# Optimization experiments

Hardware: AMD Instinct MI355X
Metric: run time of the kernel (lower is better)

Reference implementation:

```python
import jax, jax.numpy as jnp
import numpy as np

V, T, E, H, B, S = 50000, 45, 256, 512, 32, 256


def setup_inputs() -> dict:
    key = jax.random.key(0)
    ks = jax.random.split(key, 14)
    s = 0.05
    return dict(
        x=jax.random.randint(ks[0], (B, S), 0, V),
        tags=jax.random.randint(ks[1], (B, S), 0, T),
        mask=jnp.ones((B, S), dtype=bool),
        emb=jax.random.normal(ks[2], (V, E), jnp.float32),
        Wih_f=jax.random.normal(ks[3], (4 * H, E), jnp.float32) * s,
        Whh_f=jax.random.normal(ks[4], (4 * H, H), jnp.float32) * s,
        bih_f=jnp.zeros((4 * H,), jnp.float32),
        bhh_f=jnp.zeros((4 * H,), jnp.float32),
        Wih_b=jax.random.normal(ks[5], (4 * H, E), jnp.float32) * s,
        Whh_b=jax.random.normal(ks[6], (4 * H, H), jnp.float32) * s,
        bih_b=jnp.zeros((4 * H,), jnp.float32),
        bhh_b=jnp.zeros((4 * H,), jnp.float32),
        Wout=jax.random.normal(ks[7], (T, 2 * H), jnp.float32) * s,
        bout=jnp.zeros((T,), jnp.float32),
        start=jax.random.normal(ks[8], (T,), jnp.float32) * 0.1,
        end=jax.random.normal(ks[9], (T,), jnp.float32) * 0.1,
        trans=jax.random.normal(ks[10], (T, T), jnp.float32) * 0.1,
    )


def _lstm_dir(xp, Whh, reverse):
    # xp: [S, B, 4H] precomputed input projection + biases; gate order i,f,g,o (torch)
    Bn = xp.shape[1]
    Hn = Whh.shape[1]
    def step(carry, g_in):
        h, c = carry
        g = g_in + h @ Whh.T
        i, f, gg, o = jnp.split(g, 4, axis=-1)
        c = jax.nn.sigmoid(f) * c + jax.nn.sigmoid(i) * jnp.tanh(gg)
        h = jax.nn.sigmoid(o) * jnp.tanh(c)
        return (h, c), h
    init = (jnp.zeros((Bn, Hn), xp.dtype), jnp.zeros((Bn, Hn), xp.dtype))
    _, hs = jax.lax.scan(step, init, xp, reverse=reverse)
    return hs  # [S, B, H]


def _crf_nll(emissions, tags, mask, start, end, trans):
    # emissions: [B, S, T]; neg mean log-likelihood (torchcrf, reduction='mean')
    mf = mask.astype(emissions.dtype)
    em_tag = jnp.take_along_axis(emissions, tags[:, :, None], axis=2)[:, :, 0]  # [B,S]
    num = start[tags[:, 0]] + em_tag[:, 0]
    num = num + ((trans[tags[:, :-1], tags[:, 1:]] + em_tag[:, 1:]) * mf[:, 1:]).sum(1)
    seq_ends = mf.sum(1).astype(tags.dtype) - 1
    last_tags = jnp.take_along_axis(tags, seq_ends[:, None], axis=1)[:, 0]
    num = num + end[last_tags]
    def denom_step(alpha, inp):
        em_t, m_t = inp  # [B,T], [B]
        nxt = jax.nn.logsumexp(alpha[:, :, None] + trans[None, :, :] + em_t[:, None, :], axis=1)
        return jnp.where(m_t[:, None] > 0, nxt, alpha), None
    alpha0 = start[None, :] + emissions[:, 0]
    em_rest = emissions.transpose(1, 0, 2)[1:]  # [S-1, B, T]
    alpha, _ = jax.lax.scan(denom_step, alpha0, (em_rest, mf.T[1:]))
    logZ = jax.nn.logsumexp(alpha + end[None, :], axis=1)
    return -(num - logZ).mean()


def reference(x, tags, mask, emb, Wih_f, Whh_f, bih_f, bhh_f,
              Wih_b, Whh_b, bih_b, bhh_b, Wout, bout, start, end, trans):
    embeds = emb[x]                      # [B, S, E]
    xs = embeds.transpose(1, 0, 2)       # [S, B, E]
    xp_f = jnp.einsum('sbe,ge->sbg', xs, Wih_f) + bih_f + bhh_f
    hs_f = _lstm_dir(xp_f, Whh_f, False)
    xp_b = jnp.einsum('sbe,ge->sbg', xs, Wih_b) + bih_b + bhh_b
    hs_b = _lstm_dir(xp_b, Whh_b, True)
    hcat = jnp.concatenate([hs_f, hs_b], axis=-1)          # [S, B, 2H]
    emissions = jnp.einsum('sbh,th->sbt', hcat, Wout) + bout
    emissions = emissions.transpose(1, 0, 2)                # [B, S, T]
    return _crf_nll(emissions, tags, mask, start, end, trans)
```

## Files before the change

### kernel.cpp

```cpp
#include <hip/hip_runtime.h>
#include <stdint.h>

#define S_LEN 256
#define B_N 32
#define H_N 512
#define E_N 256
#define T_N 45
#define G4H 2048

typedef unsigned short u16;
typedef unsigned int u32;
typedef u16 u16x8 __attribute__((ext_vector_type(8)));
typedef u16 u16x4 __attribute__((ext_vector_type(4)));
typedef u32 u32x4 __attribute__((ext_vector_type(4)));
typedef __bf16 bf16x8 __attribute__((ext_vector_type(8)));
typedef float f32x4 __attribute__((ext_vector_type(4)));
typedef unsigned long long u64;

#define OFF_ATOK  256ull
#define OFF_WIHF  (OFF_ATOK + 4194304ull)
#define OFF_WIHB  (OFF_WIHF + 1048576ull)
#define OFF_WHHF  (OFF_WIHB + 1048576ull)
#define OFF_WHHB  (OFF_WHHF + 2097152ull)
#define OFF_WOUT  (OFF_WHHB + 2097152ull)
#define OFF_BSF   (OFF_WOUT + 98304ull)
#define OFF_BSB   (OFF_BSF + 8192ull)
#define OFF_XPF   (OFF_BSB + 8192ull)
#define OFF_XPB   (OFF_XPF + 33554432ull)
#define OFF_HSF   (OFF_XPB + 33554432ull)
#define OFF_HSB   (OFF_HSF + 8421376ull)
#define OFF_EM    (OFF_HSB + 8421376ull)
#define OFF_VAL   (OFF_EM + 1572864ull)

__device__ __forceinline__ u16 f2bf(float f) {
  union { float f; unsigned u; } v; v.f = f;
  unsigned r = v.u + 0x7FFFu + ((v.u >> 16) & 1u);
  return (u16)(r >> 16);
}
__device__ __forceinline__ float bf2f(u16 b) {
  union { unsigned u; float f; } v; v.u = ((unsigned)b) << 16;
  return v.f;
}
__device__ __forceinline__ bf16x8 ld8(const u16* p) {
  u16x8 v = *reinterpret_cast<const u16x8*>(p);
  return __builtin_bit_cast(bf16x8, v);
}
__device__ __forceinline__ void st_h8cc(u16* p, u16x4 v) {
  __hip_atomic_store(reinterpret_cast<u64*>(p), __builtin_bit_cast(u64, v),
                     __ATOMIC_RELAXED, __HIP_MEMORY_SCOPE_AGENT);
}
__device__ __forceinline__ u32x4 ld16cc(const u16* p) {
  u32x4 r;
  asm volatile("global_load_dwordx4 %0, %1, off sc0 sc1"
               : "=v"(r) : "v"(p) : "memory");
  return r;
}
__device__ __forceinline__ f32x4 mfma16(bf16x8 a, bf16x8 b, f32x4 c) {
  return __builtin_amdgcn_mfma_f32_16x16x32_bf16(a, b, c, 0, 0, 0);
}
__device__ __forceinline__ float sigm(float x) { return 1.f / (1.f + __expf(-x)); }
__device__ __forceinline__ float tanhf_(float x) {
  float ax = fabsf(x);
  float e = __expf(-2.f * ax);
  float t = 1.f - 2.f * e / (1.f + e);
  return (x < 0.f) ? -t : t;
}
__device__ __forceinline__ float wredmax(float v) {
  #pragma unroll
  for (int m = 1; m < 64; m <<= 1) v = fmaxf(v, __shfl_xor(v, m));
  return v;
}
__device__ __forceinline__ float wredsum(float v) {
  #pragma unroll
  for (int m = 1; m < 64; m <<= 1) v += __shfl_xor(v, m);
  return v;
}

__global__ void k_castA(const int* __restrict__ x, const float* __restrict__ emb,
                        u16* __restrict__ atok) {
  int idx = blockIdx.x * 256 + threadIdx.x;
  int t = idx >> 5;
  int e0 = (idx & 31) << 3;
  int s = t >> 5, b = t & 31;
  int xid = x[b * S_LEN + s];
  const float4* p = reinterpret_cast<const float4*>(emb + (size_t)xid * E_N + e0);
  float4 lo = p[0], hi = p[1];
  u16x8 o;
  o[0] = f2bf(lo.x); o[1] = f2bf(lo.y); o[2] = f2bf(lo.z); o[3] = f2bf(lo.w);
  o[4] = f2bf(hi.x); o[5] = f2bf(hi.y); o[6] = f2bf(hi.z); o[7] = f2bf(hi.w);
  *reinterpret_cast<u16x8*>(atok + (size_t)t * E_N + e0) = o;
}

__global__ void k_castW(const float* __restrict__ WihF, const float* __restrict__ WihB,
                        const float* __restrict__ WhhF, const float* __restrict__ WhhB,
                        const float* __restrict__ Wout,
                        const float* __restrict__ bihF, const float* __restrict__ bhhF,
                        const float* __restrict__ bihB, const float* __restrict__ bhhB,
                        u16* wihf, u16* wihb, u16* whhf, u16* whhb, u16* woutp,
                        float* bsf, float* bsb, u16* hsf, u16* hsb) {
  int i = blockIdx.x * 256 + threadIdx.x;
  if (i < 524288) { wihf[i] = f2bf(WihF[i]); return; }
  i -= 524288;
  if (i < 524288) { wihb[i] = f2bf(WihB[i]); return; }
  i -= 524288;
  if (i < 1048576) { whhf[i] = f2bf(WhhF[i]); return; }
  i -= 1048576;
  if (i < 1048576) { whhb[i] = f2bf(WhhB[i]); return; }
  i -= 1048576;
  if (i < 49152) {
    int n = i >> 10, k = i & 1023;
    woutp[i] = (n < T_N) ? f2bf(Wout[n * 1024 + k]) : (u16)0;
    return;
  }
  i -= 49152;
  if (i < 2048) { bsf[i] = bihF[i] + bhhF[i]; return; }
  i -= 2048;
  if (i < 2048) { bsb[i] = bihB[i] + bhhB[i]; return; }
  i -= 2048;
  if (i < 16384) { hsf[i] = 0; return; }
  i -= 16384;
  if (i < 16384) { hsb[(size_t)256 * 16384 + i] = 0; return; }
}

__global__ __launch_bounds__(256) void k_gemm_xp(
    const u16* __restrict__ atok, const u16* __restrict__ wihF, const u16* __restrict__ wihB,
    const float* __restrict__ bsF, const float* __restrict__ bsB,
    u16* __restrict__ xpF, u16* __restrict__ xpB) {
  int wid = blockIdx.x;
  int dir = wid >> 10, rem = wid & 1023;
  const int wave = threadIdx.x >> 6, lane = threadIdx.x & 63;
  const int lr = lane & 15, lh = lane >> 4;
  const int t0 = (rem >> 3) * 64;
  const int g0 = (rem & 7) * 256 + wave * 64;
  const u16* wih = dir ? wihB : wihF;
  const float* bs = dir ? bsB : bsF;
  u16* xp = dir ? xpB : xpF;
  f32x4 acc[4][4] = {};
  for (int kk = 0; kk < 8; ++kk) {
    int e = kk * 32 + lh * 8;
    bf16x8 a[4], bfr[4];
    #pragma unroll
    for (int mi = 0; mi < 4; ++mi) a[mi] = ld8(atok + (size_t)(t0 + 16 * mi + lr) * E_N + e);
    #pragma unroll
    for (int ni = 0; ni < 4; ++ni) bfr[ni] = ld8(wih + (size_t)(g0 + 16 * ni + lr) * E_N + e);
    #pragma unroll
    for (int mi = 0; mi < 4; ++mi)
      #pragma unroll
      for (int ni = 0; ni < 4; ++ni) acc[mi][ni] = mfma16(a[mi], bfr[ni], acc[mi][ni]);
  }
  #pragma unroll
  for (int ni = 0; ni < 4; ++ni) {
    int g = g0 + 16 * ni + lr;
    float bsv = bs[g];
    #pragma unroll
    for (int mi = 0; mi < 4; ++mi)
      #pragma unroll
      for (int r = 0; r < 4; ++r) {
        int t = t0 + 16 * mi + 4 * lh + r;
        xp[(size_t)t * G4H + g] = f2bf(acc[mi][ni][r] + bsv);
      }
  }
}

__global__ __launch_bounds__(128, 1) void k_lstm(
    const u16* __restrict__ whhF, const u16* __restrict__ whhB,
    const u16* __restrict__ xpF, const u16* __restrict__ xpB,
    u16* __restrict__ hsF, u16* __restrict__ hsB) {
  const int dir = blockIdx.x >> 5;
  const int w = blockIdx.x & 31;
  const int nt = threadIdx.x >> 6;
  const int lane = threadIdx.x & 63;
  const int lr = lane & 15, lh = lane >> 4;
  const u16* whh = dir ? whhB : whhF;
  const u16* xp = dir ? xpB : xpF;
  u16* hs = dir ? hsB : hsF;

  bf16x8 A[4][16];
  #pragma unroll
  for (int mt = 0; mt < 4; ++mt) {
    const u16* base = whh + (size_t)(mt * 512 + 16 * w + lr) * H_N + lh * 8;
    #pragma unroll
    for (int kk = 0; kk < 16; ++kk) A[mt][kk] = ld8(base + kk * 32);
  }
  const int b = nt * 16 + lr;
  const int j0 = 16 * w + 4 * lh;
  float cst[4] = {0.f, 0.f, 0.f, 0.f};

  for (int t = 0; t < S_LEN; ++t) {
    const int s = dir ? (S_LEN - 1 - t) : t;
    const int slot_r = dir ? (s + 1) : s;
    const int slot_w = dir ? s : (s + 1);
    u16x4 xq[4];
    const u16* xpt = xp + ((size_t)(s * B_N + b)) * G4H + j0;
    #pragma unroll
    for (int mt = 0; mt < 4; ++mt) xq[mt] = *reinterpret_cast<const u16x4*>(xpt + mt * 512);

    const u16* hp = hs + ((size_t)slot_r * B_N + b) * H_N + lh * 8;
    u32x4 raw[16];
    #pragma unroll
    for (int kk = 0; kk < 16; ++kk) raw[kk] = ld16cc(hp + kk * 32);
    asm volatile("s_waitcnt vmcnt(0)" ::: "memory");
    __builtin_amdgcn_sched_barrier(0);
    u32 pend = 0;
    #pragma unroll
    for (int kk = 0; kk < 16; ++kk)
      if (raw[kk][0] == 0xFFFFFFFFu || raw[kk][2] == 0xFFFFFFFFu) pend |= (1u << kk);
    while (__builtin_amdgcn_ballot_w64(pend != 0u)) {
      #pragma unroll
      for (int kk = 0; kk < 16; ++kk)
        if (pend & (1u << kk)) raw[kk] = ld16cc(hp + kk * 32);
      asm volatile("s_waitcnt vmcnt(0)" ::: "memory");
      __builtin_amdgcn_sched_barrier(0);
      u32 np = 0;
      #pragma unroll
      for (int kk = 0; kk < 16; ++kk)
        if ((pend & (1u << kk)) &&
            (raw[kk][0] == 0xFFFFFFFFu || raw[kk][2] == 0xFFFFFFFFu)) np |= (1u << kk);
      pend = np;
    }

    f32x4 acc[4] = {};
    #pragma unroll
    for (int kk = 0; kk < 16; ++kk) {
      bf16x8 Bf = __builtin_bit_cast(bf16x8, raw[kk]);
      #pragma unroll
      for (int mt = 0; mt < 4; ++mt) acc[mt] = mfma16(A[mt][kk], Bf, acc[mt]);
    }
    u16x4 hv;
    #pragma unroll
    for (int r = 0; r < 4; ++r) {
      float gi = acc[0][r] + bf2f(xq[0][r]);
      float gf = acc[1][r] + bf2f(xq[1][r]);
      float gg = acc[2][r] + bf2f(xq[2][r]);
      float go = acc[3][r] + bf2f(xq[3][r]);
      float c = sigm(gf) * cst[r] + sigm(gi) * tanhf_(gg);
      cst[r] = c;
      hv[r] = f2bf(sigm(go) * tanhf_(c));
    }
    st_h8cc(hs + ((size_t)slot_w * B_N + b) * H_N + j0, hv);
  }
}

__global__ __launch_bounds__(256) void k_gemm_em(
    const u16* __restrict__ hsF, const u16* __restrict__ hsB,
    const u16* __restrict__ woutp, const float* __restrict__ bout, float* __restrict__ em) {
  const int wave = threadIdx.x >> 6, lane = threadIdx.x & 63;
  const int lr = lane & 15, lh = lane >> 4;
  const int t0 = blockIdx.x * 64 + wave * 16;
  f32x4 acc[3] = {};
  for (int kk = 0; kk < 32; ++kk) {
    int k = kk * 32 + lh * 8;
    int t = t0 + lr;
    int s = t >> 5, bt = t & 31;
    const u16* ap = (kk < 16) ? (hsF + ((size_t)(s + 1) * B_N + bt) * H_N + k)
                              : (hsB + ((size_t)s * B_N + bt) * H_N + (k - 512));
    bf16x8 a = ld8(ap);
    #pragma unroll
    for (int ni = 0; ni < 3; ++ni) {
      bf16x8 bb = ld8(woutp + (size_t)(16 * ni + lr) * 1024 + k);
      acc[ni] = mfma16(a, bb, acc[ni]);
    }
  }
  #pragma unroll
  for (int ni = 0; ni < 3; ++ni) {
    int tag = 16 * ni + lr;
    float bo = (tag < T_N) ? bout[tag] : 0.f;
    #pragma unroll
    for (int r = 0; r < 4; ++r) {
      int t = t0 + 4 * lh + r;
      em[(size_t)t * 48 + tag] = acc[ni][r] + bo;
    }
  }
}

__global__ __launch_bounds__(64) void k_crf(
    const float* __restrict__ em, const int* __restrict__ tags,
    const float* __restrict__ start, const float* __restrict__ endv,
    const float* __restrict__ trans, float* __restrict__ val) {
  __shared__ float tl[T_N * T_N + 32];
  const int b = blockIdx.x;
  const int lane = threadIdx.x;
  for (int i = lane; i < T_N * T_N + 32; i += 64)
    tl[i] = (i < T_N * T_N) ? trans[i] : 0.f;
  __syncthreads();
  float acur = (lane < T_N) ? (start[lane] + em[(size_t)b * 48 + lane]) : -1e30f;
  for (int s = 1; s < S_LEN; ++s) {
    float shift = wredmax(acur);
    float emv = (lane < 48) ? em[((size_t)s * B_N + b) * 48 + lane] : 0.f;
    float s0 = 0.f, s1 = 0.f, s2 = 0.f;
    #pragma unroll
    for (int t = 0; t < T_N; t += 3) {
      s0 += __expf(__shfl(acur, t)     + tl[t * T_N + lane]       - shift);
      s1 += __expf(__shfl(acur, t + 1) + tl[(t + 1) * T_N + lane] - shift);
      s2 += __expf(__shfl(acur, t + 2) + tl[(t + 2) * T_N + lane] - shift);
    }
    acur = (lane < T_N) ? (shift + __logf(s0 + s1 + s2) + emv) : -1e30f;
  }
  float z = (lane < T_N) ? (acur + endv[lane]) : -1e30f;
  float m = wredmax(z);
  float sum = wredsum((lane < T_N) ? __expf(z - m) : 0.f);
  float logZ = m + __logf(sum);
  float np = 0.f;
  #pragma unroll
  for (int q = 0; q < 4; ++q) {
    int s = 1 + lane * 4 + q;
    if (s < S_LEN) {
      int tp = tags[b * S_LEN + s - 1], tc = tags[b * S_LEN + s];
      np += tl[tp * T_N + tc] + em[((size_t)s * B_N + b) * 48 + tc];
    }
  }
  np = wredsum(np);
  if (lane == 0) {
    int tg0 = tags[b * S_LEN], tgL = tags[b * S_LEN + S_LEN - 1];
    float num = start[tg0] + em[(size_t)b * 48 + tg0] + np + endv[tgL];
    val[b] = num - logZ;
  }
}

__global__ void k_final(const float* __restrict__ val, float* __restrict__ out) {
  int lane = threadIdx.x & 63;
  float v = (lane < B_N) ? val[lane] : 0.f;
  v = wredsum(v);
  if (threadIdx.x == 0) out[0] = -(v / (float)B_N);
}

extern "C" void kernel_launch(void* const* d_in, const int* in_sizes, int n_in,
                              void* d_out, int out_size, void* d_ws, size_t ws_size,
                              hipStream_t stream) {
  const int* x = (const int*)d_in[0];
  const int* tags = (const int*)d_in[1];
  const float* emb = (const float*)d_in[3];
  const float* WihF = (const float*)d_in[4];
  const float* WhhF = (const float*)d_in[5];
  const float* bihF = (const float*)d_in[6];
  const float* bhhF = (const float*)d_in[7];
  const float* WihB = (const float*)d_in[8];
  const float* WhhB = (const float*)d_in[9];
  const float* bihB = (const float*)d_in[10];
  const float* bhhB = (const float*)d_in[11];
  const float* Wout = (const float*)d_in[12];
  const float* bout = (const float*)d_in[13];
  const float* start = (const float*)d_in[14];
  const float* endv = (const float*)d_in[15];
  const float* trans = (const float*)d_in[16];
  float* out = (float*)d_out;
  char* ws = (char*)d_ws;

  u16* atok = (u16*)(ws + OFF_ATOK);
  u16* wihf = (u16*)(ws + OFF_WIHF);
  u16* wihb = (u16*)(ws + OFF_WIHB);
  u16* whhf = (u16*)(ws + OFF_WHHF);
  u16* whhb = (u16*)(ws + OFF_WHHB);
  u16* woutp = (u16*)(ws + OFF_WOUT);
  float* bsf = (float*)(ws + OFF_BSF);
  float* bsb = (float*)(ws + OFF_BSB);
  u16* xpf = (u16*)(ws + OFF_XPF);
  u16* xpb = (u16*)(ws + OFF_XPB);
  u16* hsf = (u16*)(ws + OFF_HSF);
  u16* hsb = (u16*)(ws + OFF_HSB);
  float* emis = (float*)(ws + OFF_EM);
  float* val = (float*)(ws + OFF_VAL);

  hipMemsetAsync(ws + OFF_HSF + 32768ull, 0xFF, 8388608ull, stream);
  hipMemsetAsync(ws + OFF_HSB, 0xFF, 8388608ull, stream);
  k_castA<<<1024, 256, 0, stream>>>(x, emb, atok);
  k_castW<<<12624, 256, 0, stream>>>(WihF, WihB, WhhF, WhhB, Wout, bihF, bhhF, bihB, bhhB,
                                     wihf, wihb, whhf, whhb, woutp, bsf, bsb, hsf, hsb);
  k_gemm_xp<<<2048, 256, 0, stream>>>(atok, wihf, wihb, bsf, bsb, xpf, xpb);
  k_lstm<<<64, 128, 0, stream>>>(whhf, whhb, xpf, xpb, hsf, hsb);
  k_gemm_em<<<128, 256, 0, stream>>>(hsf, hsb, woutp, bout, emis);
  k_crf<<<32, 64, 0, stream>>>(emis, tags, start, endv, trans, val);
  k_final<<<1, 64, 0, stream>>>(val, out);
}
```

Before: 1.530 ms.

## Pin LSTM workgroups per direction to one XCC and exchange hidden state through L2

The LSTM kernel now launches many workgroups, and each one reads its hardware XCC id. Each XCC claims one direction by atomic counter, so the 32 workgroups of a direction can share L2. Those workgroups publish and poll the hidden state with L2-scope (sc0) stores and loads instead of system-coherent ones, which cuts the per-step cross-die sync latency. As a fallback, a mirror buffer is written with agent-scope stores, and timed-out or unplaced workgroups poll that. The cost is extra memsets, a duplicate hidden-state store on every step, and correctness that rests on XCC-id placement and timeout heuristics.

```diff
diff --git a/kernel.cpp b/kernel.cpp
--- a/kernel.cpp
+++ b/kernel.cpp
@@ -17,6 +17,7 @@
 typedef float f32x4 __attribute__((ext_vector_type(4)));
 typedef unsigned long long u64;
 
+#define OFF_CLM   0ull
 #define OFF_ATOK  256ull
 #define OFF_WIHF  (OFF_ATOK + 4194304ull)
 #define OFF_WIHB  (OFF_WIHF + 1048576ull)
@@ -29,7 +30,9 @@
 #define OFF_XPB   (OFF_XPF + 33554432ull)
 #define OFF_HSF   (OFF_XPB + 33554432ull)
 #define OFF_HSB   (OFF_HSF + 8421376ull)
-#define OFF_EM    (OFF_HSB + 8421376ull)
+#define OFF_HMF   (OFF_HSB + 8421376ull)
+#define OFF_HMB   (OFF_HMF + 8421376ull)
+#define OFF_EM    (OFF_HMB + 8421376ull)
 #define OFF_VAL   (OFF_EM + 1572864ull)
 
 __device__ __forceinline__ u16 f2bf(float f) {
@@ -45,9 +48,19 @@
   u16x8 v = *reinterpret_cast<const u16x8*>(p);
   return __builtin_bit_cast(bf16x8, v);
 }
+__device__ __forceinline__ void st_h8_l2(u16* p, u16x4 v) {
+  __hip_atomic_store(reinterpret_cast<u64*>(p), __builtin_bit_cast(u64, v),
+                     __ATOMIC_RELAXED, __HIP_MEMORY_SCOPE_WORKGROUP);
+}
 __device__ __forceinline__ void st_h8cc(u16* p, u16x4 v) {
   __hip_atomic_store(reinterpret_cast<u64*>(p), __builtin_bit_cast(u64, v),
                      __ATOMIC_RELAXED, __HIP_MEMORY_SCOPE_AGENT);
+}
+__device__ __forceinline__ u32x4 ld16l2(const u16* p) {
+  u32x4 r;
+  asm volatile("global_load_dwordx4 %0, %1, off sc0"
+               : "=v"(r) : "v"(p) : "memory");
+  return r;
 }
 __device__ __forceinline__ u32x4 ld16cc(const u16* p) {
   u32x4 r;
@@ -97,7 +110,8 @@
                         const float* __restrict__ bihF, const float* __restrict__ bhhF,
                         const float* __restrict__ bihB, const float* __restrict__ bhhB,
                         u16* wihf, u16* wihb, u16* whhf, u16* whhb, u16* woutp,
-                        float* bsf, float* bsb, u16* hsf, u16* hsb) {
+                        float* bsf, float* bsb, u16* hsf, u16* hsb,
+                        u16* hmf, u16* hmb) {
   int i = blockIdx.x * 256 + threadIdx.x;
   if (i < 524288) { wihf[i] = f2bf(WihF[i]); return; }
   i -= 524288;
@@ -120,6 +134,10 @@
   if (i < 16384) { hsf[i] = 0; return; }
   i -= 16384;
   if (i < 16384) { hsb[(size_t)256 * 16384 + i] = 0; return; }
+  i -= 16384;
+  if (i < 16384) { hmf[i] = 0; return; }
+  i -= 16384;
+  if (i < 16384) { hmb[(size_t)256 * 16384 + i] = 0; return; }
 }
 
 __global__ __launch_bounds__(256) void k_gemm_xp(
@@ -165,15 +183,49 @@
 __global__ __launch_bounds__(128, 1) void k_lstm(
     const u16* __restrict__ whhF, const u16* __restrict__ whhB,
     const u16* __restrict__ xpF, const u16* __restrict__ xpB,
-    u16* __restrict__ hsF, u16* __restrict__ hsB) {
-  const int dir = blockIdx.x >> 5;
-  const int w = blockIdx.x & 31;
+    u16* __restrict__ hsF, u16* __restrict__ hsB,
+    u16* __restrict__ hmF, u16* __restrict__ hmB, int* claim) {
+  __shared__ int sh_dir, sh_w, sh_fast;
+  if (threadIdx.x == 0) {
+    u32 xcc;
+    asm volatile("s_getreg_b32 %0, hwreg(20, 0, 32)" : "=s"(xcc));
+    xcc &= 7u;
+    int dir = -1, w = -1, fast = 0;
+    if (xcc <= 1u) {
+      int r = __hip_atomic_fetch_add(&claim[xcc], 1, __ATOMIC_RELAXED,
+                                     __HIP_MEMORY_SCOPE_AGENT);
+      if (r < 32) { dir = (int)xcc; w = r; fast = 1; }
+    }
+    if (dir < 0) {
+      int r2 = __hip_atomic_fetch_add(&claim[2], 1, __ATOMIC_RELAXED,
+                                      __HIP_MEMORY_SCOPE_AGENT);
+      if (r2 < 64) {
+        int bd = r2 >> 5, bw = r2 & 31;
+        u64 t0 = __builtin_amdgcn_s_memrealtime();
+        for (;;) {
+          int c = __hip_atomic_load(&claim[bd], __ATOMIC_RELAXED,
+                                    __HIP_MEMORY_SCOPE_AGENT);
+          if (c >= 32) break;
+          if (__builtin_amdgcn_s_memrealtime() - t0 > 50000ull) {
+            dir = bd; w = bw; fast = 0; break;
+          }
+          __builtin_amdgcn_s_sleep(8);
+        }
+      }
+    }
+    sh_dir = dir; sh_w = w; sh_fast = fast;
+  }
+  __syncthreads();
+  const int dir = sh_dir, w = sh_w, fast = sh_fast;
+  if (dir < 0) return;
+
   const int nt = threadIdx.x >> 6;
   const int lane = threadIdx.x & 63;
   const int lr = lane & 15, lh = lane >> 4;
   const u16* whh = dir ? whhB : whhF;
   const u16* xp = dir ? xpB : xpF;
   u16* hs = dir ? hsB : hsF;
+  u16* hm = dir ? hmB : hmF;
 
   bf16x8 A[4][16];
   #pragma unroll
@@ -195,20 +247,34 @@
     #pragma unroll
     for (int mt = 0; mt < 4; ++mt) xq[mt] = *reinterpret_cast<const u16x4*>(xpt + mt * 512);
 
-    const u16* hp = hs + ((size_t)slot_r * B_N + b) * H_N + lh * 8;
+    const size_t rbase = ((size_t)slot_r * B_N + b) * H_N + lh * 8;
+    const u16* hpl = hs + rbase;
+    const u16* hpm = hm + rbase;
     u32x4 raw[16];
-    #pragma unroll
-    for (int kk = 0; kk < 16; ++kk) raw[kk] = ld16cc(hp + kk * 32);
+    if (fast) {
+      #pragma unroll
+      for (int kk = 0; kk < 16; ++kk) raw[kk] = ld16l2(hpl + kk * 32);
+    } else {
+      #pragma unroll
+      for (int kk = 0; kk < 16; ++kk) raw[kk] = ld16cc(hpm + kk * 32);
+    }
     asm volatile("s_waitcnt vmcnt(0)" ::: "memory");
     __builtin_amdgcn_sched_barrier(0);
     u32 pend = 0;
     #pragma unroll
     for (int kk = 0; kk < 16; ++kk)
       if (raw[kk][0] == 0xFFFFFFFFu || raw[kk][2] == 0xFFFFFFFFu) pend |= (1u << kk);
+    int round = 1;
     while (__builtin_amdgcn_ballot_w64(pend != 0u)) {
-      #pragma unroll
-      for (int kk = 0; kk < 16; ++kk)
-        if (pend & (1u << kk)) raw[kk] = ld16cc(hp + kk * 32);
+      if (fast && round < 4) {
+        #pragma unroll
+        for (int kk = 0; kk < 16; ++kk)
+          if (pend & (1u << kk)) raw[kk] = ld16l2(hpl + kk * 32);
+      } else {
+        #pragma unroll
+        for (int kk = 0; kk < 16; ++kk)
+          if (pend & (1u << kk)) raw[kk] = ld16cc(hpm + kk * 32);
+      }
       asm volatile("s_waitcnt vmcnt(0)" ::: "memory");
       __builtin_amdgcn_sched_barrier(0);
       u32 np = 0;
@@ -217,6 +283,7 @@
         if ((pend & (1u << kk)) &&
             (raw[kk][0] == 0xFFFFFFFFu || raw[kk][2] == 0xFFFFFFFFu)) np |= (1u << kk);
       pend = np;
+      ++round;
     }
 
     f32x4 acc[4] = {};
@@ -237,7 +304,9 @@
       cst[r] = c;
       hv[r] = f2bf(sigm(go) * tanhf_(c));
     }
-    st_h8cc(hs + ((size_t)slot_w * B_N + b) * H_N + j0, hv);
+    const size_t wbase = ((size_t)slot_w * B_N + b) * H_N + j0;
+    st_h8_l2(hs + wbase, hv);
+    st_h8cc(hm + wbase, hv);
   }
 }
 
@@ -358,16 +427,23 @@
   u16* xpb = (u16*)(ws + OFF_XPB);
   u16* hsf = (u16*)(ws + OFF_HSF);
   u16* hsb = (u16*)(ws + OFF_HSB);
+  u16* hmf = (u16*)(ws + OFF_HMF);
+  u16* hmb = (u16*)(ws + OFF_HMB);
   float* emis = (float*)(ws + OFF_EM);
   float* val = (float*)(ws + OFF_VAL);
 
+  hipMemsetAsync(ws + OFF_CLM, 0, 256, stream);
   hipMemsetAsync(ws + OFF_HSF + 32768ull, 0xFF, 8388608ull, stream);
   hipMemsetAsync(ws + OFF_HSB, 0xFF, 8388608ull, stream);
+  hipMemsetAsync(ws + OFF_HMF + 32768ull, 0xFF, 8388608ull, stream);
+  hipMemsetAsync(ws + OFF_HMB, 0xFF, 8388608ull, stream);
   k_castA<<<1024, 256, 0, stream>>>(x, emb, atok);
-  k_castW<<<12624, 256, 0, stream>>>(WihF, WihB, WhhF, WhhB, Wout, bihF, bhhF, bihB, bhhB,
-                                     wihf, wihb, whhf, whhb, woutp, bsf, bsb, hsf, hsb);
+  k_castW<<<12752, 256, 0, stream>>>(WihF, WihB, WhhF, WhhB, Wout, bihF, bhhF, bihB, bhhB,
+                                     wihf, wihb, whhf, whhb, woutp, bsf, bsb, hsf, hsb,
+                                     hmf, hmb);
   k_gemm_xp<<<2048, 256, 0, stream>>>(atok, wihf, wihb, bsf, bsb, xpf, xpb);
-  k_lstm<<<64, 128, 0, stream>>>(whhf, whhb, xpf, xpb, hsf, hsb);
+  k_lstm<<<768, 128, 0, stream>>>(whhf, whhb, xpf, xpb, hsf, hsb, hmf, hmb,
+                                  (int*)(ws + OFF_CLM));
   k_gemm_em<<<128, 256, 0, stream>>>(hsf, hsb, woutp, bout, emis);
   k_crf<<<32, 64, 0, stream>>>(emis, tags, start, endv, trans, val);
   k_final<<<1, 64, 0, stream>>>(val, out);
```

Result: slower. 2.287 ms (+49.4%).

## Overlap input-projection GEMM with LSTM recurrence via sentinel-polled fused kernel

Applied to the files above, without the earlier changes.

The xp GEMM blocks move into the LSTM kernel as extra workgroups. The recurrent blocks poll xp values for a 0xFF sentinel written by a memset, so the input projection overlaps the serial recurrence instead of running before it. The cast kernels are merged, k_final is replaced by an atomicAdd in the CRF kernel, and the CRF emission load is prefetched. This trades a large 64MB sentinel memset and spin-polling with cache-bypassing loads for fewer launches and overlapped work. Correctness also relies on the 64 recurrent blocks being scheduled first and on the sentinel never matching a real value.

```diff
diff --git a/kernel.cpp b/kernel.cpp
--- a/kernel.cpp
+++ b/kernel.cpp
@@ -13,6 +13,7 @@
 typedef u16 u16x8 __attribute__((ext_vector_type(8)));
 typedef u16 u16x4 __attribute__((ext_vector_type(4)));
 typedef u32 u32x4 __attribute__((ext_vector_type(4)));
+typedef u32 u32x2 __attribute__((ext_vector_type(2)));
 typedef __bf16 bf16x8 __attribute__((ext_vector_type(8)));
 typedef float f32x4 __attribute__((ext_vector_type(4)));
 typedef unsigned long long u64;
@@ -30,7 +31,6 @@
 #define OFF_HSF   (OFF_XPB + 33554432ull)
 #define OFF_HSB   (OFF_HSF + 8421376ull)
 #define OFF_EM    (OFF_HSB + 8421376ull)
-#define OFF_VAL   (OFF_EM + 1572864ull)
 
 __device__ __forceinline__ u16 f2bf(float f) {
   union { float f; unsigned u; } v; v.f = f;
@@ -51,9 +51,19 @@
 }
 __device__ __forceinline__ u32x4 ld16cc(const u16* p) {
   u32x4 r;
-  asm volatile("global_load_dwordx4 %0, %1, off sc0 sc1"
+  asm volatile("global_load_dwordx4 %0, %1, off sc1"
                : "=v"(r) : "v"(p) : "memory");
   return r;
+}
+__device__ __forceinline__ u32x2 ld8cc(const u16* p) {
+  u32x2 r;
+  asm volatile("global_load_dwordx2 %0, %1, off sc1"
+               : "=v"(r) : "v"(p) : "memory");
+  return r;
+}
+__device__ __forceinline__ void st2cc(u16* p, u32 v) {
+  asm volatile("global_store_short %0, %1, off sc1"
+               :: "v"(p), "v"(v) : "memory");
 }
 __device__ __forceinline__ f32x4 mfma16(bf16x8 a, bf16x8 b, f32x4 c) {
   return __builtin_amdgcn_mfma_f32_16x16x32_bf16(a, b, c, 0, 0, 0);
@@ -76,29 +86,31 @@
   return v;
 }
 
-__global__ void k_castA(const int* __restrict__ x, const float* __restrict__ emb,
-                        u16* __restrict__ atok) {
-  int idx = blockIdx.x * 256 + threadIdx.x;
-  int t = idx >> 5;
-  int e0 = (idx & 31) << 3;
-  int s = t >> 5, b = t & 31;
-  int xid = x[b * S_LEN + s];
-  const float4* p = reinterpret_cast<const float4*>(emb + (size_t)xid * E_N + e0);
-  float4 lo = p[0], hi = p[1];
-  u16x8 o;
-  o[0] = f2bf(lo.x); o[1] = f2bf(lo.y); o[2] = f2bf(lo.z); o[3] = f2bf(lo.w);
-  o[4] = f2bf(hi.x); o[5] = f2bf(hi.y); o[6] = f2bf(hi.z); o[7] = f2bf(hi.w);
-  *reinterpret_cast<u16x8*>(atok + (size_t)t * E_N + e0) = o;
-}
-
-__global__ void k_castW(const float* __restrict__ WihF, const float* __restrict__ WihB,
-                        const float* __restrict__ WhhF, const float* __restrict__ WhhB,
-                        const float* __restrict__ Wout,
-                        const float* __restrict__ bihF, const float* __restrict__ bhhF,
-                        const float* __restrict__ bihB, const float* __restrict__ bhhB,
-                        u16* wihf, u16* wihb, u16* whhf, u16* whhb, u16* woutp,
-                        float* bsf, float* bsb, u16* hsf, u16* hsb) {
-  int i = blockIdx.x * 256 + threadIdx.x;
+__global__ void k_castAW(const int* __restrict__ x, const float* __restrict__ emb,
+                         u16* __restrict__ atok,
+                         const float* __restrict__ WihF, const float* __restrict__ WihB,
+                         const float* __restrict__ WhhF, const float* __restrict__ WhhB,
+                         const float* __restrict__ Wout,
+                         const float* __restrict__ bihF, const float* __restrict__ bhhF,
+                         const float* __restrict__ bihB, const float* __restrict__ bhhB,
+                         u16* wihf, u16* wihb, u16* whhf, u16* whhb, u16* woutp,
+                         float* bsf, float* bsb, u16* hsf, u16* hsb) {
+  int bid = blockIdx.x;
+  if (bid < 1024) {
+    int idx = bid * 256 + threadIdx.x;
+    int t = idx >> 5;
+    int e0 = (idx & 31) << 3;
+    int s = t >> 5, b = t & 31;
+    int xid = x[b * S_LEN + s];
+    const float4* p = reinterpret_cast<const float4*>(emb + (size_t)xid * E_N + e0);
+    float4 lo = p[0], hi = p[1];
+    u16x8 o;
+    o[0] = f2bf(lo.x); o[1] = f2bf(lo.y); o[2] = f2bf(lo.z); o[3] = f2bf(lo.w);
+    o[4] = f2bf(hi.x); o[5] = f2bf(hi.y); o[6] = f2bf(hi.z); o[7] = f2bf(hi.w);
+    *reinterpret_cast<u16x8*>(atok + (size_t)t * E_N + e0) = o;
+    return;
+  }
+  int i = (bid - 1024) * 256 + threadIdx.x;
   if (i < 524288) { wihf[i] = f2bf(WihF[i]); return; }
   i -= 524288;
   if (i < 524288) { wihb[i] = f2bf(WihB[i]); return; }
@@ -122,50 +134,52 @@
   if (i < 16384) { hsb[(size_t)256 * 16384 + i] = 0; return; }
 }
 
-__global__ __launch_bounds__(256) void k_gemm_xp(
-    const u16* __restrict__ atok, const u16* __restrict__ wihF, const u16* __restrict__ wihB,
+__global__ __launch_bounds__(128, 1) void k_fused(
+    const u16* __restrict__ whhF, const u16* __restrict__ whhB,
+    const u16* __restrict__ atok,
+    const u16* __restrict__ wihF, const u16* __restrict__ wihB,
     const float* __restrict__ bsF, const float* __restrict__ bsB,
-    u16* __restrict__ xpF, u16* __restrict__ xpB) {
-  int wid = blockIdx.x;
-  int dir = wid >> 10, rem = wid & 1023;
-  const int wave = threadIdx.x >> 6, lane = threadIdx.x & 63;
-  const int lr = lane & 15, lh = lane >> 4;
-  const int t0 = (rem >> 3) * 64;
-  const int g0 = (rem & 7) * 256 + wave * 64;
-  const u16* wih = dir ? wihB : wihF;
-  const float* bs = dir ? bsB : bsF;
-  u16* xp = dir ? xpB : xpF;
-  f32x4 acc[4][4] = {};
-  for (int kk = 0; kk < 8; ++kk) {
-    int e = kk * 32 + lh * 8;
-    bf16x8 a[4], bfr[4];
-    #pragma unroll
-    for (int mi = 0; mi < 4; ++mi) a[mi] = ld8(atok + (size_t)(t0 + 16 * mi + lr) * E_N + e);
-    #pragma unroll
-    for (int ni = 0; ni < 4; ++ni) bfr[ni] = ld8(wih + (size_t)(g0 + 16 * ni + lr) * E_N + e);
-    #pragma unroll
-    for (int mi = 0; mi < 4; ++mi)
-      #pragma unroll
-      for (int ni = 0; ni < 4; ++ni) acc[mi][ni] = mfma16(a[mi], bfr[ni], acc[mi][ni]);
-  }
-  #pragma unroll
-  for (int ni = 0; ni < 4; ++ni) {
-    int g = g0 + 16 * ni + lr;
-    float bsv = bs[g];
-    #pragma unroll
-    for (int mi = 0; mi < 4; ++mi)
-      #pragma unroll
-      for (int r = 0; r < 4; ++r) {
-        int t = t0 + 16 * mi + 4 * lh + r;
-        xp[(size_t)t * G4H + g] = f2bf(acc[mi][ni][r] + bsv);
-      }
-  }
-}
-
-__global__ __launch_bounds__(128, 1) void k_lstm(
-    const u16* __restrict__ whhF, const u16* __restrict__ whhB,
-    const u16* __restrict__ xpF, const u16* __restrict__ xpB,
+    u16* __restrict__ xpF, u16* __restrict__ xpB,
     u16* __restrict__ hsF, u16* __restrict__ hsB) {
+  if (blockIdx.x >= 64) {
+    int j = (int)blockIdx.x - 64;
+    int dir = j & 1, idx = j >> 1;
+    int tIdx = idx >> 4, gIdx = idx & 15;
+    if (dir) tIdx = 127 - tIdx;
+    const int wave = threadIdx.x >> 6, lane = threadIdx.x & 63;
+    const int lr = lane & 15, lh = lane >> 4;
+    const int t0 = tIdx * 64;
+    const int g0 = gIdx * 128 + wave * 64;
+    const u16* wih = dir ? wihB : wihF;
+    const float* bs = dir ? bsB : bsF;
+    u16* xp = dir ? xpB : xpF;
+    f32x4 acc[4][4] = {};
+    for (int kk = 0; kk < 8; ++kk) {
+      int e = kk * 32 + lh * 8;
+      bf16x8 a[4], bfr[4];
+      #pragma unroll
+      for (int mi = 0; mi < 4; ++mi) a[mi] = ld8(atok + (size_t)(t0 + 16 * mi + lr) * E_N + e);
+      #pragma unroll
+      for (int ni = 0; ni < 4; ++ni) bfr[ni] = ld8(wih + (size_t)(g0 + 16 * ni + lr) * E_N + e);
+      #pragma unroll
+      for (int mi = 0; mi < 4; ++mi)
+        #pragma unroll
+        for (int ni = 0; ni < 4; ++ni) acc[mi][ni] = mfma16(a[mi], bfr[ni], acc[mi][ni]);
+    }
+    #pragma unroll
+    for (int ni = 0; ni < 4; ++ni) {
+      int g = g0 + 16 * ni + lr;
+      float bsv = bs[g];
+      #pragma unroll
+      for (int mi = 0; mi < 4; ++mi)
+        #pragma unroll
+        for (int r = 0; r < 4; ++r) {
+          int t = t0 + 16 * mi + 4 * lh + r;
+          st2cc(xp + (size_t)t * G4H + g, (u32)f2bf(acc[mi][ni][r] + bsv));
+        }
+    }
+    return;
+  }
   const int dir = blockIdx.x >> 5;
   const int w = blockIdx.x & 31;
   const int nt = threadIdx.x >> 6;
@@ -190,10 +204,11 @@
     const int s = dir ? (S_LEN - 1 - t) : t;
     const int slot_r = dir ? (s + 1) : s;
     const int slot_w = dir ? s : (s + 1);
-    u16x4 xq[4];
+
+    u32x2 xqr[4];
     const u16* xpt = xp + ((size_t)(s * B_N + b)) * G4H + j0;
     #pragma unroll
-    for (int mt = 0; mt < 4; ++mt) xq[mt] = *reinterpret_cast<const u16x4*>(xpt + mt * 512);
+    for (int mt = 0; mt < 4; ++mt) xqr[mt] = ld8cc(xpt + mt * 512);
 
     const u16* hp = hs + ((size_t)slot_r * B_N + b) * H_N + lh * 8;
     u32x4 raw[16];
@@ -206,6 +221,7 @@
     for (int kk = 0; kk < 16; ++kk)
       if (raw[kk][0] == 0xFFFFFFFFu || raw[kk][2] == 0xFFFFFFFFu) pend |= (1u << kk);
     while (__builtin_amdgcn_ballot_w64(pend != 0u)) {
+      __builtin_amdgcn_s_sleep(1);
       #pragma unroll
       for (int kk = 0; kk < 16; ++kk)
         if (pend & (1u << kk)) raw[kk] = ld16cc(hp + kk * 32);
@@ -226,13 +242,37 @@
       #pragma unroll
       for (int mt = 0; mt < 4; ++mt) acc[mt] = mfma16(A[mt][kk], Bf, acc[mt]);
     }
+
+    for (;;) {
+      u32 xbad = 0;
+      #pragma unroll
+      for (int mt = 0; mt < 4; ++mt) {
+        #pragma unroll
+        for (int d = 0; d < 2; ++d) {
+          u32 wv = xqr[mt][d];
+          xbad |= ((wv & 0xFFFFu) == 0xFFFFu) | ((wv >> 16) == 0xFFFFu);
+        }
+      }
+      if (!__builtin_amdgcn_ballot_w64(xbad != 0u)) break;
+      __builtin_amdgcn_s_sleep(1);
+      #pragma unroll
+      for (int mt = 0; mt < 4; ++mt) xqr[mt] = ld8cc(xpt + mt * 512);
+      asm volatile("s_waitcnt vmcnt(0)" ::: "memory");
+      __builtin_amdgcn_sched_barrier(0);
+    }
+
     u16x4 hv;
     #pragma unroll
     for (int r = 0; r < 4; ++r) {
-      float gi = acc[0][r] + bf2f(xq[0][r]);
-      float gf = acc[1][r] + bf2f(xq[1][r]);
-      float gg = acc[2][r] + bf2f(xq[2][r]);
-      float go = acc[3][r] + bf2f(xq[3][r]);
+      u32 w0 = xqr[0][r >> 1], w1 = xqr[1][r >> 1], w2 = xqr[2][r >> 1], w3 = xqr[3][r >> 1];
+      u16 x0 = (r & 1) ? (u16)(w0 >> 16) : (u16)(w0 & 0xFFFFu);
+      u16 x1 = (r & 1) ? (u16)(w1 >> 16) : (u16)(w1 & 0xFFFFu);
+      u16 x2 = (r & 1) ? (u16)(w2 >> 16) : (u16)(w2 & 0xFFFFu);
+      u16 x3 = (r & 1) ? (u16)(w3 >> 16) : (u16)(w3 & 0xFFFFu);
+      float gi = acc[0][r] + bf2f(x0);
+      float gf = acc[1][r] + bf2f(x1);
+      float gg = acc[2][r] + bf2f(x2);
+      float go = acc[3][r] + bf2f(x3);
       float c = sigm(gf) * cst[r] + sigm(gi) * tanhf_(gg);
       cst[r] = c;
       hv[r] = f2bf(sigm(go) * tanhf_(c));
@@ -276,7 +316,7 @@
 __global__ __launch_bounds__(64) void k_crf(
     const float* __restrict__ em, const int* __restrict__ tags,
     const float* __restrict__ start, const float* __restrict__ endv,
-    const float* __restrict__ trans, float* __restrict__ val) {
+    const float* __restrict__ trans, float* __restrict__ out) {
   __shared__ float tl[T_N * T_N + 32];
   const int b = blockIdx.x;
   const int lane = threadIdx.x;
@@ -284,9 +324,12 @@
     tl[i] = (i < T_N * T_N) ? trans[i] : 0.f;
   __syncthreads();
   float acur = (lane < T_N) ? (start[lane] + em[(size_t)b * 48 + lane]) : -1e30f;
+  float emv_next = (lane < 48) ? em[((size_t)(1 * B_N + b)) * 48 + lane] : 0.f;
   for (int s = 1; s < S_LEN; ++s) {
     float shift = wredmax(acur);
-    float emv = (lane < 48) ? em[((size_t)s * B_N + b) * 48 + lane] : 0.f;
+    float emv = emv_next;
+    if (s < S_LEN - 1)
+      emv_next = (lane < 48) ? em[((size_t)((s + 1) * B_N + b)) * 48 + lane] : 0.f;
     float s0 = 0.f, s1 = 0.f, s2 = 0.f;
     #pragma unroll
     for (int t = 0; t < T_N; t += 3) {
@@ -313,15 +356,8 @@
   if (lane == 0) {
     int tg0 = tags[b * S_LEN], tgL = tags[b * S_LEN + S_LEN - 1];
     float num = start[tg0] + em[(size_t)b * 48 + tg0] + np + endv[tgL];
-    val[b] = num - logZ;
-  }
-}
-
-__global__ void k_final(const float* __restrict__ val, float* __restrict__ out) {
-  int lane = threadIdx.x & 63;
-  float v = (lane < B_N) ? val[lane] : 0.f;
-  v = wredsum(v);
-  if (threadIdx.x == 0) out[0] = -(v / (float)B_N);
+    atomicAdd(out, -(num - logZ) / (float)B_N);
+  }
 }
 
 extern "C" void kernel_launch(void* const* d_in, const int* in_sizes, int n_in,
@@ -359,16 +395,15 @@
   u16* hsf = (u16*)(ws + OFF_HSF);
   u16* hsb = (u16*)(ws + OFF_HSB);
   float* emis = (float*)(ws + OFF_EM);
-  float* val = (float*)(ws + OFF_VAL);
-
-  hipMemsetAsync(ws + OFF_HSF + 32768ull, 0xFF, 8388608ull, stream);
-  hipMemsetAsync(ws + OFF_HSB, 0xFF, 8388608ull, stream);
-  k_castA<<<1024, 256, 0, stream>>>(x, emb, atok);
-  k_castW<<<12624, 256, 0, stream>>>(WihF, WihB, WhhF, WhhB, Wout, bihF, bhhF, bihB, bhhB,
-                                     wihf, wihb, whhf, whhb, woutp, bsf, bsb, hsf, hsb);
-  k_gemm_xp<<<2048, 256, 0, stream>>>(atok, wihf, wihb, bsf, bsb, xpf, xpb);
-  k_lstm<<<64, 128, 0, stream>>>(whhf, whhb, xpf, xpb, hsf, hsb);
+
+  hipMemsetAsync(out, 0, sizeof(float), stream);
+  hipMemsetAsync(ws + OFF_HSF + 32768ull, 0xFF, 16777216ull, stream);
+  hipMemsetAsync(ws + OFF_XPF, 0xFF, 67108864ull, stream);
+  k_castAW<<<13648, 256, 0, stream>>>(x, emb, atok, WihF, WihB, WhhF, WhhB, Wout,
+                                      bihF, bhhF, bihB, bhhB,
+                                      wihf, wihb, whhf, whhb, woutp, bsf, bsb, hsf, hsb);
+  k_fused<<<4160, 128, 0, stream>>>(whhf, whhb, atok, wihf, wihb, bsf, bsb,
+                                    xpf, xpb, hsf, hsb);
   k_gemm_em<<<128, 256, 0, stream>>>(hsf, hsb, woutp, bout, emis);
-  k_crf<<<32, 64, 0, stream>>>(emis, tags, start, endv, trans, val);
-  k_final<<<1, 64, 0, stream>>>(val, out);
-}
+  k_crf<<<32, 64, 0, stream>>>(emis, tags, start, endv, trans, out);
+}
```

New measurement: 1.501 ms. About the same (-1.9%).
